# Performance work log

Hardware: AMD Instinct MI355X
Metric: run time of the kernel (lower is better)

## Reference

```python
import jax, jax.numpy as jnp
import numpy as np

B, N, T, D, H = 32, 64, 16, 256, 256  # batch, actors, frames, feat dim, hidden_dim


def setup_inputs() -> dict:
    key = jax.random.key(0)
    ks = jax.random.split(key, 6)
    s = lambda fan: 1.0 / np.sqrt(fan)
    return {
        "x": jax.random.normal(ks[0], (B, N, T, D), jnp.float32),
        "W1_t": jax.random.normal(ks[1], (T * D, H), jnp.float32) * s(T * D),
        "b1_t": jnp.zeros((H,), jnp.float32),
        "W2_t": jax.random.normal(ks[2], (H, H), jnp.float32) * s(H),
        "b2_t": jnp.zeros((H,), jnp.float32),
        "W1_i": jax.random.normal(ks[3], (2 * H, H), jnp.float32) * s(2 * H),
        "b1_i": jnp.zeros((H,), jnp.float32),
        "W2_i": jax.random.normal(ks[4], (H, H), jnp.float32) * s(H),
        "b2_i": jnp.zeros((H,), jnp.float32),
    }


def reference(x, W1_t, b1_t, W2_t, b2_t, W1_i, b1_i, W2_i, b2_i):
    b, n, t, d = x.shape
    # STTR_trans output is immediately detached in the original; modeled as
    # identity + stop_gradient (view(N,B,T,-1) then view-back is a no-op on data).
    pf = jax.lax.stop_gradient(x)  # [B, N, T, D]

    # time_track_projection: MLP(T*D -> H -> H), ReLU between layers, no BN, eval dropout.
    h = jax.nn.relu(pf.reshape(b * n, t * d) @ W1_t + b1_t)
    person_feature = (h @ W2_t + b2_t).reshape(b, n, -1)  # [B, N, H]

    # relation_indexes: row-major enumeration of ordered pairs (i, j), j != i.
    # tem1 row N*i+j holds feature i, tem2 row N*i+j holds feature j.
    ii, jj = np.nonzero(~np.eye(n, dtype=bool))  # each [N*(N-1)], row-major order
    pair = jnp.concatenate(
        [person_feature[:, ii, :], person_feature[:, jj, :]], axis=-1
    )  # [B, N*(N-1), 2H] -- gather avoids materializing the full N*N grid

    # interaction_track_projection: MLP(2H -> H -> H)
    hi = jax.nn.relu(pair @ W1_i + b1_i)
    relation_feature = hi @ W2_i + b2_i  # [B, N*(N-1), H]

    return relation_feature, pf, person_feature
```

## Files before the change

### kernel.cpp

```cpp
#include <hip/hip_runtime.h>
#include <stdint.h>

typedef unsigned short u16;
typedef __attribute__((ext_vector_type(4))) float f32x4;
typedef __attribute__((ext_vector_type(8))) short bf16x8;
typedef __attribute__((ext_vector_type(4))) unsigned short u16x4;

#define DEV static __device__ __forceinline__

DEV u16 f2bf(float f) {
  union { float f; uint32_t u; } v; v.f = f;
  uint32_t u = v.u;
  return (u16)((u + 0x7FFFu + ((u >> 16) & 1u)) >> 16);
}

DEV float bf2f(u16 u) {
  union { uint32_t u; float f; } v; v.u = ((uint32_t)u) << 16;
  return v.f;
}

__global__ __launch_bounds__(256) void k_pre(const float* __restrict__ x,
                                             float* __restrict__ pf,
                                             u16* __restrict__ xb,
                                             const float* __restrict__ W1t,
                                             const float* __restrict__ W2t,
                                             const float* __restrict__ W1i,
                                             const float* __restrict__ W2i,
                                             const float* __restrict__ b2t,
                                             const float* __restrict__ b1i,
                                             u16* __restrict__ W1T,
                                             u16* __restrict__ W2iT,
                                             u16* __restrict__ WcatT,
                                             float* __restrict__ biascat) {
  __shared__ u16 tile[64][65];
  __shared__ float col[256];
  int b = blockIdx.x;
  int t = threadIdx.x;
  if (b < 4096) {
    int i = b * 256 + t;
    #pragma unroll
    for (int h = 0; h < 2; ++h) {
      f32x4 v = *(const f32x4*)(x + i * 8 + h * 4);
      *(f32x4*)(pf + i * 8 + h * 4) = v;
      u16x4 o;
      #pragma unroll
      for (int e = 0; e < 4; ++e) o[e] = f2bf(v[e]);
      *(u16x4*)(xb + i * 8 + h * 4) = o;
    }
    return;
  }
  b -= 4096;
  if (b < 272) {
    const float* in;
    u16* out;
    int R, C, bb;
    if (b < 256) { in = W1t; out = W1T; R = 4096; C = 256; bb = b; }
    else         { in = W2i; out = W2iT; R = 256;  C = 256; bb = b - 256; }
    int tr = (bb >> 2) * 64, tc = (bb & 3) * 64;
    int lr = t & 63;
    #pragma unroll
    for (int it = 0; it < 16; ++it) {
      int r = it * 4 + (t >> 6);
      tile[r][lr] = f2bf(in[(tr + r) * C + tc + lr]);
    }
    __syncthreads();
    #pragma unroll
    for (int it = 0; it < 16; ++it) {
      int c = it * 4 + (t >> 6);
      out[(tc + c) * R + tr + lr] = tile[lr][c];
    }
    return;
  }
  if (b < 1040) {
    int n = b - 272;
    int k = t;
    if (n < 256) {
      WcatT[n * 256 + k] = f2bf(W2t[k * 256 + n]);
      return;
    }
    int off = (n < 512) ? 0 : 256;
    int c = n & 255;
    col[k] = W1i[(off + k) * 256 + c];
    __syncthreads();
    const float* wrow = W2t + k * 256;
    float acc = 0.f;
    #pragma unroll 4
    for (int m = 0; m < 256; ++m) acc += wrow[m] * col[m];
    WcatT[n * 256 + k] = f2bf(acc);
    return;
  }
  int n = (b - 1040) * 256 + t;
  float v;
  if (n < 256) {
    v = b2t[n];
  } else {
    int off = (n < 512) ? 0 : 256;
    int c = n & 255;
    float acc = (n < 512) ? 0.f : b1i[c];
    for (int k = 0; k < 256; ++k) acc += b2t[k] * W1i[(off + k) * 256 + c];
    v = acc;
  }
  biascat[n] = v;
}

__global__ __launch_bounds__(256) void k_gemm1(const u16* __restrict__ A,
                                               const u16* __restrict__ BT,
                                               u16* __restrict__ part) {
  int w = threadIdx.x >> 6, l = threadIdx.x & 63;
  int m0 = blockIdx.x * 32;
  int n0 = w * 64;
  int k0 = blockIdx.y * 256 + ((l >> 4) * 8);
  const u16* pa0 = A + (m0 + (l & 15)) * 4096 + k0;
  const u16* pb0 = BT + (n0 + (l & 15)) * 4096 + k0;
  f32x4 acc[2][4] = {};
  #pragma unroll 2
  for (int ks = 0; ks < 8; ++ks) {
    bf16x8 a[2], bfr[4];
    #pragma unroll
    for (int mf = 0; mf < 2; ++mf)
      a[mf] = *(const bf16x8*)(pa0 + mf * 16 * 4096 + ks * 32);
    #pragma unroll
    for (int nf = 0; nf < 4; ++nf)
      bfr[nf] = *(const bf16x8*)(pb0 + nf * 16 * 4096 + ks * 32);
    #pragma unroll
    for (int mf = 0; mf < 2; ++mf)
      #pragma unroll
      for (int nf = 0; nf < 4; ++nf)
        acc[mf][nf] = __builtin_amdgcn_mfma_f32_16x16x32_bf16(bfr[nf], a[mf], acc[mf][nf], 0, 0, 0);
  }
  u16* out = part + blockIdx.y * (2048 * 256);
  #pragma unroll
  for (int mf = 0; mf < 2; ++mf) {
    int row = m0 + mf * 16 + (l & 15);
    #pragma unroll
    for (int nf = 0; nf < 4; ++nf) {
      int colv = n0 + nf * 16 + ((l >> 4) * 4);
      u16x4 o;
      #pragma unroll
      for (int r = 0; r < 4; ++r) o[r] = f2bf(acc[mf][nf][r]);
      *(u16x4*)(out + row * 256 + colv) = o;
    }
  }
}

__global__ __launch_bounds__(256) void k_reduce_h(const u16* __restrict__ part,
                                                  const float* __restrict__ b1t,
                                                  u16* __restrict__ hb) {
  int i = blockIdx.x * 256 + threadIdx.x;
  int e = i * 4;
  f32x4 s = {};
  #pragma unroll
  for (int z = 0; z < 16; ++z) {
    u16x4 p = *(const u16x4*)(part + z * (2048 * 256) + e);
    #pragma unroll
    for (int r = 0; r < 4; ++r) s[r] += bf2f(p[r]);
  }
  f32x4 bb = *(const f32x4*)(b1t + (e & 255));
  u16x4 o;
  #pragma unroll
  for (int r = 0; r < 4; ++r) o[r] = f2bf(fmaxf(s[r] + bb[r], 0.f));
  *(u16x4*)(hb + e) = o;
}

__global__ __launch_bounds__(256) void k_gemm3(const u16* __restrict__ A,
                                               const u16* __restrict__ BT,
                                               const float* __restrict__ biascat,
                                               float* __restrict__ person,
                                               float* __restrict__ Apr,
                                               float* __restrict__ Bpr) {
  int w = threadIdx.x >> 6, l = threadIdx.x & 63;
  int row = blockIdx.x * 64 + w * 16 + (l & 15);
  int coln = blockIdx.y * 64;
  int k0 = (l >> 4) * 8;
  const u16* pa = A + row * 256 + k0;
  const u16* pb0 = BT + (coln + (l & 15)) * 256 + k0;
  f32x4 acc[4] = {};
  #pragma unroll
  for (int ks = 0; ks < 8; ++ks) {
    bf16x8 a = *(const bf16x8*)(pa + ks * 32);
    #pragma unroll
    for (int nf = 0; nf < 4; ++nf) {
      bf16x8 b = *(const bf16x8*)(pb0 + nf * 16 * 256 + ks * 32);
      acc[nf] = __builtin_amdgcn_mfma_f32_16x16x32_bf16(b, a, acc[nf], 0, 0, 0);
    }
  }
  float* dst;
  int cbase = coln;
  if (coln < 256) { dst = person; }
  else if (coln < 512) { dst = Apr; cbase = coln - 256; }
  else { dst = Bpr; cbase = coln - 512; }
  #pragma unroll
  for (int nf = 0; nf < 4; ++nf) {
    int lc = nf * 16 + ((l >> 4) * 4);
    f32x4 bias4 = *(const f32x4*)(biascat + coln + lc);
    *(f32x4*)(dst + row * 256 + cbase + lc) = acc[nf] + bias4;
  }
}

__global__ __launch_bounds__(512, 2) void k_pair_gemm(const float* __restrict__ Apr,
                                                      const float* __restrict__ Bpr,
                                                      const u16* __restrict__ W2iT,
                                                      const float* __restrict__ b2i,
                                                      float* __restrict__ rel) {
  __shared__ u16 hi[128 * 264];
  int t = threadIdx.x;
  int lane = t & 63;
  int R0 = blockIdx.x * 128;
  #pragma unroll
  for (int it = 0; it < 16; ++it) {
    int r = it * 8 + (t >> 6);
    int R = R0 + r;
    int b = R / 4032;
    int q = R - b * 4032;
    int i = q / 63;
    int rem = q - i * 63;
    int j = rem + (rem >= i ? 1 : 0);
    f32x4 va = *(const f32x4*)(Apr + (b * 64 + i) * 256 + lane * 4);
    f32x4 vb = *(const f32x4*)(Bpr + (b * 64 + j) * 256 + lane * 4);
    u16x4 o;
    #pragma unroll
    for (int e = 0; e < 4; ++e) o[e] = f2bf(fmaxf(va[e] + vb[e], 0.f));
    *(u16x4*)(&hi[r * 264 + lane * 4]) = o;
  }
  __syncthreads();
  int wid = t >> 6;
  int wr = wid >> 2, wc = wid & 3;
  f32x4 acc[4][4] = {};
  int arow0 = wr * 64 + (lane & 15);
  int koff = (lane >> 4) * 8;
  const u16* pb0 = W2iT + (wc * 64 + (lane & 15)) * 256 + koff;
  #pragma unroll 2
  for (int ks = 0; ks < 8; ++ks) {
    bf16x8 a[4], bfr[4];
    #pragma unroll
    for (int mf = 0; mf < 4; ++mf)
      a[mf] = *(const bf16x8*)(&hi[(arow0 + mf * 16) * 264 + ks * 32 + koff]);
    #pragma unroll
    for (int nf = 0; nf < 4; ++nf)
      bfr[nf] = *(const bf16x8*)(pb0 + nf * 16 * 256 + ks * 32);
    #pragma unroll
    for (int mf = 0; mf < 4; ++mf)
      #pragma unroll
      for (int nf = 0; nf < 4; ++nf)
        acc[mf][nf] = __builtin_amdgcn_mfma_f32_16x16x32_bf16(bfr[nf], a[mf], acc[mf][nf], 0, 0, 0);
  }
  f32x4 bias4[4];
  #pragma unroll
  for (int nf = 0; nf < 4; ++nf)
    bias4[nf] = *(const f32x4*)(b2i + wc * 64 + nf * 16 + ((lane >> 4) * 4));
  #pragma unroll
  for (int mf = 0; mf < 4; ++mf) {
    int row = R0 + wr * 64 + mf * 16 + (lane & 15);
    #pragma unroll
    for (int nf = 0; nf < 4; ++nf) {
      int gc = wc * 64 + nf * 16 + ((lane >> 4) * 4);
      *(f32x4*)(rel + row * 256 + gc) = acc[mf][nf] + bias4[nf];
    }
  }
}


extern "C" void kernel_launch(void* const* d_in, const int* in_sizes, int n_in,
                              void* d_out, int out_size, void* d_ws, size_t ws_size,
                              hipStream_t stream) {
  const float* x   = (const float*)d_in[0];
  const float* W1t = (const float*)d_in[1];
  const float* b1t = (const float*)d_in[2];
  const float* W2t = (const float*)d_in[3];
  const float* b2t = (const float*)d_in[4];
  const float* W1i = (const float*)d_in[5];
  const float* b1i = (const float*)d_in[6];
  const float* W2i = (const float*)d_in[7];
  const float* b2i = (const float*)d_in[8];

  float* out = (float*)d_out;
  float* rel = out;
  float* pf = out + 33030144;
  float* person = out + 41418752;

  char* ws = (char*)d_ws;
  u16*   x_bf    = (u16*)(ws + 0);
  u16*   W1T     = (u16*)(ws + 16777216);
  u16*   WcatT   = (u16*)(ws + 18874368);
  u16*   W2iT    = (u16*)(ws + 19267584);
  float* biascat = (float*)(ws + 19398656);
  u16*   h_bf    = (u16*)(ws + 19402752);
  float* Apr     = (float*)(ws + 20451328);
  float* Bpr     = (float*)(ws + 22548480);
  u16*   part    = (u16*)(ws + 24645632);

  k_pre<<<5139, 256, 0, stream>>>(x, pf, x_bf, W1t, W2t, W1i, W2i, b2t, b1i,
                                  W1T, W2iT, WcatT, biascat);
  k_gemm1<<<dim3(64, 16), 256, 0, stream>>>(x_bf, W1T, part);
  k_reduce_h<<<512, 256, 0, stream>>>(part, b1t, h_bf);
  k_gemm3<<<dim3(32, 12), 256, 0, stream>>>(h_bf, WcatT, biascat, person, Apr, Bpr);
  k_pair_gemm<<<1008, 512, 0, stream>>>(Apr, Bpr, W2iT, b2i, rel);
}
```

Baseline: 145.6 us.

## Fuse x copy and bf16 conversion into first GEMM via LDS staging

The fp32 x read, the pf copy and the bf16 conversion now happen inside the first GEMM kernel, which stages the converted A tile in shared memory. This removes the separate pass that wrote and reread a bf16 copy of x through global memory. The split-K factor is halved (512-wide K slices, 8 partials), which halves the partial-sum traffic in the reduce kernel. In exchange the grid has fewer blocks, and each block must finish its staging load before any MFMA work starts.

```diff
diff --git a/kernel.cpp b/kernel.cpp
--- a/kernel.cpp
+++ b/kernel.cpp
@@ -19,37 +19,20 @@
   return v.f;
 }
 
-__global__ __launch_bounds__(256) void k_pre(const float* __restrict__ x,
-                                             float* __restrict__ pf,
-                                             u16* __restrict__ xb,
-                                             const float* __restrict__ W1t,
-                                             const float* __restrict__ W2t,
-                                             const float* __restrict__ W1i,
-                                             const float* __restrict__ W2i,
-                                             const float* __restrict__ b2t,
-                                             const float* __restrict__ b1i,
-                                             u16* __restrict__ W1T,
-                                             u16* __restrict__ W2iT,
-                                             u16* __restrict__ WcatT,
-                                             float* __restrict__ biascat) {
+__global__ __launch_bounds__(256) void k_prep(const float* __restrict__ W1t,
+                                              const float* __restrict__ W2t,
+                                              const float* __restrict__ W1i,
+                                              const float* __restrict__ W2i,
+                                              const float* __restrict__ b2t,
+                                              const float* __restrict__ b1i,
+                                              u16* __restrict__ W1T,
+                                              u16* __restrict__ W2iT,
+                                              u16* __restrict__ WcatT,
+                                              float* __restrict__ biascat) {
   __shared__ u16 tile[64][65];
   __shared__ float col[256];
   int b = blockIdx.x;
   int t = threadIdx.x;
-  if (b < 4096) {
-    int i = b * 256 + t;
-    #pragma unroll
-    for (int h = 0; h < 2; ++h) {
-      f32x4 v = *(const f32x4*)(x + i * 8 + h * 4);
-      *(f32x4*)(pf + i * 8 + h * 4) = v;
-      u16x4 o;
-      #pragma unroll
-      for (int e = 0; e < 4; ++e) o[e] = f2bf(v[e]);
-      *(u16x4*)(xb + i * 8 + h * 4) = o;
-    }
-    return;
-  }
-  b -= 4096;
   if (b < 272) {
     const float* in;
     u16* out;
@@ -103,22 +86,41 @@
   biascat[n] = v;
 }
 
-__global__ __launch_bounds__(256) void k_gemm1(const u16* __restrict__ A,
-                                               const u16* __restrict__ BT,
-                                               u16* __restrict__ part) {
-  int w = threadIdx.x >> 6, l = threadIdx.x & 63;
+__global__ __launch_bounds__(256) void k_gemm1f(const float* __restrict__ x,
+                                                float* __restrict__ pf,
+                                                const u16* __restrict__ BT,
+                                                u16* __restrict__ part) {
+  __shared__ u16 As[32][520];
+  int t = threadIdx.x;
   int m0 = blockIdx.x * 32;
+  int k0 = blockIdx.y * 512;
+  {
+    int row = t >> 3;
+    int cb = (t & 7) * 4;
+    const float* src = x + (m0 + row) * 4096 + k0;
+    float* dst = pf + (m0 + row) * 4096 + k0;
+    #pragma unroll
+    for (int j = 0; j < 16; ++j) {
+      f32x4 v = *(const f32x4*)(src + cb + j * 32);
+      *(f32x4*)(dst + cb + j * 32) = v;
+      u16x4 o;
+      #pragma unroll
+      for (int e = 0; e < 4; ++e) o[e] = f2bf(v[e]);
+      *(u16x4*)(&As[row][cb + j * 32]) = o;
+    }
+  }
+  __syncthreads();
+  int w = t >> 6, l = t & 63;
   int n0 = w * 64;
-  int k0 = blockIdx.y * 256 + ((l >> 4) * 8);
-  const u16* pa0 = A + (m0 + (l & 15)) * 4096 + k0;
-  const u16* pb0 = BT + (n0 + (l & 15)) * 4096 + k0;
+  int koff = (l >> 4) * 8;
+  const u16* pb0 = BT + (n0 + (l & 15)) * 4096 + k0 + koff;
+  int ar = l & 15;
   f32x4 acc[2][4] = {};
-  #pragma unroll 2
-  for (int ks = 0; ks < 8; ++ks) {
+  for (int ks = 0; ks < 16; ++ks) {
     bf16x8 a[2], bfr[4];
     #pragma unroll
     for (int mf = 0; mf < 2; ++mf)
-      a[mf] = *(const bf16x8*)(pa0 + mf * 16 * 4096 + ks * 32);
+      a[mf] = *(const bf16x8*)(&As[ar + mf * 16][koff + ks * 32]);
     #pragma unroll
     for (int nf = 0; nf < 4; ++nf)
       bfr[nf] = *(const bf16x8*)(pb0 + nf * 16 * 4096 + ks * 32);
@@ -150,7 +152,7 @@
   int e = i * 4;
   f32x4 s = {};
   #pragma unroll
-  for (int z = 0; z < 16; ++z) {
+  for (int z = 0; z < 8; ++z) {
     u16x4 p = *(const u16x4*)(part + z * (2048 * 256) + e);
     #pragma unroll
     for (int r = 0; r < 4; ++r) s[r] += bf2f(p[r]);
@@ -279,19 +281,18 @@
   float* person = out + 41418752;
 
   char* ws = (char*)d_ws;
-  u16*   x_bf    = (u16*)(ws + 0);
-  u16*   W1T     = (u16*)(ws + 16777216);
-  u16*   WcatT   = (u16*)(ws + 18874368);
-  u16*   W2iT    = (u16*)(ws + 19267584);
-  float* biascat = (float*)(ws + 19398656);
-  u16*   h_bf    = (u16*)(ws + 19402752);
-  float* Apr     = (float*)(ws + 20451328);
-  float* Bpr     = (float*)(ws + 22548480);
-  u16*   part    = (u16*)(ws + 24645632);
-
-  k_pre<<<5139, 256, 0, stream>>>(x, pf, x_bf, W1t, W2t, W1i, W2i, b2t, b1i,
-                                  W1T, W2iT, WcatT, biascat);
-  k_gemm1<<<dim3(64, 16), 256, 0, stream>>>(x_bf, W1T, part);
+  u16*   W1T     = (u16*)(ws + 0);
+  u16*   WcatT   = (u16*)(ws + 2097152);
+  u16*   W2iT    = (u16*)(ws + 2490368);
+  float* biascat = (float*)(ws + 2621440);
+  u16*   h_bf    = (u16*)(ws + 2625536);
+  float* Apr     = (float*)(ws + 3674112);
+  float* Bpr     = (float*)(ws + 5771264);
+  u16*   part    = (u16*)(ws + 7868416);
+
+  k_prep<<<1043, 256, 0, stream>>>(W1t, W2t, W1i, W2i, b2t, b1i,
+                                   W1T, W2iT, WcatT, biascat);
+  k_gemm1f<<<dim3(64, 8), 256, 0, stream>>>(x, pf, W1T, part);
   k_reduce_h<<<512, 256, 0, stream>>>(part, b1t, h_bf);
   k_gemm3<<<dim3(32, 12), 256, 0, stream>>>(h_bf, WcatT, biascat, person, Apr, Bpr);
   k_pair_gemm<<<1008, 512, 0, stream>>>(Apr, Bpr, W2iT, b2i, rel);
```

Result: faster. 119.6 us (-17.9%).
